# Kernel optimization log

Measured on AMD Instinct MI355X. Metric: run time of the kernel, lower is better.

## Reference

```python
import jax, jax.numpy as jnp
import numpy as np

N = 32
R = 128  # num_regions
F = 128  # num_features


def setup_inputs() -> dict:
    key = jax.random.key(0)
    k1, k2, k3, k4 = jax.random.split(key, 4)
    x1 = jax.random.normal(k1, (N, R * F), dtype=jnp.float32)
    x2 = jax.random.normal(k2, (N, R * F), dtype=jnp.float32)
    sigma = jax.random.normal(k3, (1,), dtype=jnp.float32) * 100.0
    mean = jax.random.normal(k4, (1,), dtype=jnp.float32)
    return {"x1": x1, "x2": x2, "sigma": sigma, "mean": mean}


def reference(x1, x2, sigma, mean):
    # (N, R, 1, F) - (N, 1, R, F) - mean -> (N, R, R, F)
    a = x1.reshape(N, R, 1, F)
    b = x2.reshape(N, 1, R, F)
    diff = a - b - mean  # mean is shape (1,), broadcasts over F
    distance_squared = jnp.sum(diff * diff, axis=-1)  # (N, R, R)
    kernel_value = jnp.exp(-distance_squared / (2.0 * sigma[0] ** 2))
    return jax.nn.softmax(kernel_value, axis=-1)
```

## Files before the change

### kernel.cpp

```cpp
#include <hip/hip_runtime.h>

#define NB 32
#define RR 128
#define FF 128
#define FT 32
#define SB 132

__global__ __launch_bounds__(256) void gauss_fused(const float* __restrict__ x1,
                                                   const float* __restrict__ x2,
                                                   const float* __restrict__ sigma,
                                                   const float* __restrict__ mean,
                                                   float* __restrict__ out) {
  __shared__ __align__(16) float sh_b[FT * SB];
  __shared__ __align__(16) float sh_a[8 * FF];

  const int bid = blockIdx.x;
  const int n = bid >> 4;
  const int i0 = (bid & 15) << 3;
  const int tid = threadIdx.x;
  const int tx = tid & 31;
  const int ty = tid >> 5;

  const float mval = mean[0];
  const float sg = sigma[0];
  const float cneg = -1.0f / (2.0f * sg * sg);

  {
    const float4 v = ((const float4*)(x1 + (size_t)(n * RR + i0) * FF))[tid];
    ((float4*)sh_a)[tid] = make_float4(v.x - mval, v.y - mval, v.z - mval, v.w - mval);
  }

  const float* __restrict__ x2base = x2 + (size_t)n * RR * FF;
  const int jj = tid >> 3;
  const int fo = (tid & 7) << 2;

  float acc0 = 0.f, acc1 = 0.f, acc2 = 0.f, acc3 = 0.f;
  const int j0 = tx << 2;
  const float* __restrict__ arow = sh_a + ty * FF;

  for (int t = 0; t < FF / FT; ++t) {
    const int ftw = t * FT;
    __syncthreads();
#pragma unroll
    for (int p = 0; p < 4; ++p) {
      const int j = jj + p * 32;
      const float4 v = *(const float4*)(x2base + (size_t)j * FF + ftw + fo);
      sh_b[(fo + 0) * SB + j] = v.x;
      sh_b[(fo + 1) * SB + j] = v.y;
      sh_b[(fo + 2) * SB + j] = v.z;
      sh_b[(fo + 3) * SB + j] = v.w;
    }
    __syncthreads();

#pragma unroll
    for (int f = 0; f < FT; ++f) {
      const float4 b = *(const float4*)(sh_b + f * SB + j0);
      const float a = arow[ftw + f];
      float d;
      d = a - b.x; acc0 = fmaf(d, d, acc0);
      d = a - b.y; acc1 = fmaf(d, d, acc1);
      d = a - b.z; acc2 = fmaf(d, d, acc2);
      d = a - b.w; acc3 = fmaf(d, d, acc3);
    }
  }

  const float k0 = __expf(acc0 * cneg);
  const float k1 = __expf(acc1 * cneg);
  const float k2 = __expf(acc2 * cneg);
  const float k3 = __expf(acc3 * cneg);

  float mx = fmaxf(fmaxf(k0, k1), fmaxf(k2, k3));
#pragma unroll
  for (int off = 16; off >= 1; off >>= 1) mx = fmaxf(mx, __shfl_xor(mx, off, 64));
  const float e0 = __expf(k0 - mx);
  const float e1 = __expf(k1 - mx);
  const float e2 = __expf(k2 - mx);
  const float e3 = __expf(k3 - mx);
  float ssum = e0 + e1 + e2 + e3;
#pragma unroll
  for (int off = 16; off >= 1; off >>= 1) ssum += __shfl_xor(ssum, off, 64);
  const float r = 1.0f / ssum;

  *(float4*)(out + (size_t)(n * RR + i0 + ty) * RR + j0) =
      make_float4(e0 * r, e1 * r, e2 * r, e3 * r);
}

extern "C" void kernel_launch(void* const* d_in, const int* in_sizes, int n_in,
                              void* d_out, int out_size, void* d_ws, size_t ws_size,
                              hipStream_t stream) {
  const float* x1 = (const float*)d_in[0];
  const float* x2 = (const float*)d_in[1];
  const float* sigma = (const float*)d_in[2];
  const float* mean = (const float*)d_in[3];
  float* out = (float*)d_out;
  (void)d_ws; (void)ws_size;

  gauss_fused<<<dim3(NB * 16), dim3(256), 0, stream>>>(x1, x2, sigma, mean, out);
}
```

Before: 69.42 us.

## Double-buffer x2 tiles in LDS with register prefetch and vectorized A reads

Turns the single shared-memory tile of x2 into two buffers. The next feature slice is prefetched into registers while the current slice is being computed, which overlaps the global-load latency with the math and cuts one barrier per iteration. It also reads the x1 row from shared memory as float4 vectors instead of scalars. The cost is more registers and twice the LDS for the B tile, which could lower occupancy.

```diff
diff --git a/kernel.cpp b/kernel.cpp
--- a/kernel.cpp
+++ b/kernel.cpp
@@ -11,7 +11,7 @@
                                                    const float* __restrict__ sigma,
                                                    const float* __restrict__ mean,
                                                    float* __restrict__ out) {
-  __shared__ __align__(16) float sh_b[FT * SB];
+  __shared__ __align__(16) float sh_b[2][FT * SB];
   __shared__ __align__(16) float sh_a[8 * FF];
 
   const int bid = blockIdx.x;
@@ -25,42 +25,87 @@
   const float sg = sigma[0];
   const float cneg = -1.0f / (2.0f * sg * sg);
 
+  const float* __restrict__ x2base = x2 + (size_t)n * RR * FF;
+  const int jj = tid >> 3;
+  const int fo = (tid & 7) << 2;
+
+  float4 p0 = *(const float4*)(x2base + (size_t)(jj + 0) * FF + fo);
+  float4 p1 = *(const float4*)(x2base + (size_t)(jj + 32) * FF + fo);
+  float4 p2 = *(const float4*)(x2base + (size_t)(jj + 64) * FF + fo);
+  float4 p3 = *(const float4*)(x2base + (size_t)(jj + 96) * FF + fo);
   {
     const float4 v = ((const float4*)(x1 + (size_t)(n * RR + i0) * FF))[tid];
     ((float4*)sh_a)[tid] = make_float4(v.x - mval, v.y - mval, v.z - mval, v.w - mval);
   }
-
-  const float* __restrict__ x2base = x2 + (size_t)n * RR * FF;
-  const int jj = tid >> 3;
-  const int fo = (tid & 7) << 2;
+  {
+    float* dst = sh_b[0];
+    dst[(fo + 0) * SB + (jj + 0)] = p0.x;
+    dst[(fo + 1) * SB + (jj + 0)] = p0.y;
+    dst[(fo + 2) * SB + (jj + 0)] = p0.z;
+    dst[(fo + 3) * SB + (jj + 0)] = p0.w;
+    dst[(fo + 0) * SB + (jj + 32)] = p1.x;
+    dst[(fo + 1) * SB + (jj + 32)] = p1.y;
+    dst[(fo + 2) * SB + (jj + 32)] = p1.z;
+    dst[(fo + 3) * SB + (jj + 32)] = p1.w;
+    dst[(fo + 0) * SB + (jj + 64)] = p2.x;
+    dst[(fo + 1) * SB + (jj + 64)] = p2.y;
+    dst[(fo + 2) * SB + (jj + 64)] = p2.z;
+    dst[(fo + 3) * SB + (jj + 64)] = p2.w;
+    dst[(fo + 0) * SB + (jj + 96)] = p3.x;
+    dst[(fo + 1) * SB + (jj + 96)] = p3.y;
+    dst[(fo + 2) * SB + (jj + 96)] = p3.z;
+    dst[(fo + 3) * SB + (jj + 96)] = p3.w;
+  }
+  __syncthreads();
 
   float acc0 = 0.f, acc1 = 0.f, acc2 = 0.f, acc3 = 0.f;
   const int j0 = tx << 2;
-  const float* __restrict__ arow = sh_a + ty * FF;
-
-  for (int t = 0; t < FF / FT; ++t) {
-    const int ftw = t * FT;
-    __syncthreads();
-#pragma unroll
-    for (int p = 0; p < 4; ++p) {
-      const int j = jj + p * 32;
-      const float4 v = *(const float4*)(x2base + (size_t)j * FF + ftw + fo);
-      sh_b[(fo + 0) * SB + j] = v.x;
-      sh_b[(fo + 1) * SB + j] = v.y;
-      sh_b[(fo + 2) * SB + j] = v.z;
-      sh_b[(fo + 3) * SB + j] = v.w;
-    }
-    __syncthreads();
+  int buf = 0;
 
 #pragma unroll
-    for (int f = 0; f < FT; ++f) {
-      const float4 b = *(const float4*)(sh_b + f * SB + j0);
-      const float a = arow[ftw + f];
-      float d;
-      d = a - b.x; acc0 = fmaf(d, d, acc0);
-      d = a - b.y; acc1 = fmaf(d, d, acc1);
-      d = a - b.z; acc2 = fmaf(d, d, acc2);
-      d = a - b.w; acc3 = fmaf(d, d, acc3);
+  for (int t = 0; t < FF / FT; ++t) {
+    float4 q[4];
+    if (t < 3) {
+      const float* src = x2base + (size_t)(t + 1) * FT + fo;
+#pragma unroll
+      for (int p = 0; p < 4; ++p)
+        q[p] = *(const float4*)(src + (size_t)(jj + 32 * p) * FF);
+    }
+
+    float4 a4[8];
+    {
+      const float4* asrc = (const float4*)(sh_a + ty * FF + t * FT);
+#pragma unroll
+      for (int fq = 0; fq < 8; ++fq) a4[fq] = asrc[fq];
+    }
+
+    const float* __restrict__ bb = sh_b[buf];
+#pragma unroll
+    for (int fq = 0; fq < 8; ++fq) {
+      const float4 av = a4[fq];
+#pragma unroll
+      for (int k = 0; k < 4; ++k) {
+        const float a = (k == 0) ? av.x : (k == 1) ? av.y : (k == 2) ? av.z : av.w;
+        const float4 b = *(const float4*)(bb + (fq * 4 + k) * SB + j0);
+        float d;
+        d = a - b.x; acc0 = fmaf(d, d, acc0);
+        d = a - b.y; acc1 = fmaf(d, d, acc1);
+        d = a - b.z; acc2 = fmaf(d, d, acc2);
+        d = a - b.w; acc3 = fmaf(d, d, acc3);
+      }
+    }
+
+    if (t < 3) {
+      float* dst = sh_b[buf ^ 1];
+#pragma unroll
+      for (int p = 0; p < 4; ++p) {
+        dst[(fo + 0) * SB + (jj + 32 * p)] = q[p].x;
+        dst[(fo + 1) * SB + (jj + 32 * p)] = q[p].y;
+        dst[(fo + 2) * SB + (jj + 32 * p)] = q[p].z;
+        dst[(fo + 3) * SB + (jj + 32 * p)] = q[p].w;
+      }
+      __syncthreads();
+      buf ^= 1;
     }
   }
 
```

Result: slower. 145.7 us (+109.8%).

## Stage full x2 slice once per block and compute two output rows per thread

Applied to the files above, without the earlier changes.

Each block now loads the whole 128x128 x2 slice for its batch into shared memory in one pass with a single barrier, replacing the four-chunk loop that synchronised twice per chunk. Each block handles 16 rows instead of 8, so each thread keeps two sets of accumulators and reuses every shared-memory b load for two rows. x1 values are read as float4 to cut LDS instructions. In exchange, shared memory grows to about 74KB per block and the grid halves to 256 blocks, which lowers occupancy and may leave some compute units idle on a large GPU.

```diff
diff --git a/kernel.cpp b/kernel.cpp
--- a/kernel.cpp
+++ b/kernel.cpp
@@ -3,7 +3,6 @@
 #define NB 32
 #define RR 128
 #define FF 128
-#define FT 32
 #define SB 132
 
 __global__ __launch_bounds__(256) void gauss_fused(const float* __restrict__ x1,
@@ -11,12 +10,12 @@
                                                    const float* __restrict__ sigma,
                                                    const float* __restrict__ mean,
                                                    float* __restrict__ out) {
-  __shared__ __align__(16) float sh_b[FT * SB];
-  __shared__ __align__(16) float sh_a[8 * FF];
+  __shared__ __align__(16) float sh_b[FF * SB];
+  __shared__ __align__(16) float sh_a[16 * FF];
 
   const int bid = blockIdx.x;
-  const int n = bid >> 4;
-  const int i0 = (bid & 15) << 3;
+  const int n = bid >> 3;
+  const int i0 = (bid & 7) << 4;
   const int tid = threadIdx.x;
   const int tx = tid & 31;
   const int ty = tid >> 5;
@@ -25,64 +24,98 @@
   const float sg = sigma[0];
   const float cneg = -1.0f / (2.0f * sg * sg);
 
+  const float* __restrict__ x2base = x2 + (size_t)n * RR * FF;
+
   {
-    const float4 v = ((const float4*)(x1 + (size_t)(n * RR + i0) * FF))[tid];
-    ((float4*)sh_a)[tid] = make_float4(v.x - mval, v.y - mval, v.z - mval, v.w - mval);
+    const float4* asrc = (const float4*)(x1 + (size_t)(n * RR + i0) * FF);
+    const float4 v0 = asrc[tid];
+    const float4 v1 = asrc[tid + 256];
+    ((float4*)sh_a)[tid] = make_float4(v0.x - mval, v0.y - mval, v0.z - mval, v0.w - mval);
+    ((float4*)sh_a)[tid + 256] = make_float4(v1.x - mval, v1.y - mval, v1.z - mval, v1.w - mval);
   }
 
-  const float* __restrict__ x2base = x2 + (size_t)n * RR * FF;
   const int jj = tid >> 3;
   const int fo = (tid & 7) << 2;
-
-  float acc0 = 0.f, acc1 = 0.f, acc2 = 0.f, acc3 = 0.f;
-  const int j0 = tx << 2;
-  const float* __restrict__ arow = sh_a + ty * FF;
-
-  for (int t = 0; t < FF / FT; ++t) {
-    const int ftw = t * FT;
-    __syncthreads();
+#pragma unroll
+  for (int fc = 0; fc < 4; ++fc) {
+    const int f0 = (fc << 5) + fo;
 #pragma unroll
     for (int p = 0; p < 4; ++p) {
-      const int j = jj + p * 32;
-      const float4 v = *(const float4*)(x2base + (size_t)j * FF + ftw + fo);
-      sh_b[(fo + 0) * SB + j] = v.x;
-      sh_b[(fo + 1) * SB + j] = v.y;
-      sh_b[(fo + 2) * SB + j] = v.z;
-      sh_b[(fo + 3) * SB + j] = v.w;
+      const int j = jj + (p << 5);
+      const float4 v = *(const float4*)(x2base + (size_t)j * FF + f0);
+      sh_b[(f0 + 0) * SB + j] = v.x;
+      sh_b[(f0 + 1) * SB + j] = v.y;
+      sh_b[(f0 + 2) * SB + j] = v.z;
+      sh_b[(f0 + 3) * SB + j] = v.w;
     }
-    __syncthreads();
+  }
+  __syncthreads();
 
+  float acc00 = 0.f, acc01 = 0.f, acc02 = 0.f, acc03 = 0.f;
+  float acc10 = 0.f, acc11 = 0.f, acc12 = 0.f, acc13 = 0.f;
+  const int j0 = tx << 2;
+  const float* __restrict__ arow0 = sh_a + ty * FF;
+  const float* __restrict__ arow1 = sh_a + (ty + 8) * FF;
+
+#pragma unroll 4
+  for (int fq = 0; fq < 32; ++fq) {
+    const float4 a0 = *(const float4*)(arow0 + (fq << 2));
+    const float4 a1 = *(const float4*)(arow1 + (fq << 2));
 #pragma unroll
-    for (int f = 0; f < FT; ++f) {
-      const float4 b = *(const float4*)(sh_b + f * SB + j0);
-      const float a = arow[ftw + f];
+    for (int c = 0; c < 4; ++c) {
+      const float4 b = *(const float4*)(sh_b + ((fq << 2) + c) * SB + j0);
+      const float a0c = (c == 0) ? a0.x : (c == 1) ? a0.y : (c == 2) ? a0.z : a0.w;
+      const float a1c = (c == 0) ? a1.x : (c == 1) ? a1.y : (c == 2) ? a1.z : a1.w;
       float d;
-      d = a - b.x; acc0 = fmaf(d, d, acc0);
-      d = a - b.y; acc1 = fmaf(d, d, acc1);
-      d = a - b.z; acc2 = fmaf(d, d, acc2);
-      d = a - b.w; acc3 = fmaf(d, d, acc3);
+      d = a0c - b.x; acc00 = fmaf(d, d, acc00);
+      d = a0c - b.y; acc01 = fmaf(d, d, acc01);
+      d = a0c - b.z; acc02 = fmaf(d, d, acc02);
+      d = a0c - b.w; acc03 = fmaf(d, d, acc03);
+      d = a1c - b.x; acc10 = fmaf(d, d, acc10);
+      d = a1c - b.y; acc11 = fmaf(d, d, acc11);
+      d = a1c - b.z; acc12 = fmaf(d, d, acc12);
+      d = a1c - b.w; acc13 = fmaf(d, d, acc13);
     }
   }
 
-  const float k0 = __expf(acc0 * cneg);
-  const float k1 = __expf(acc1 * cneg);
-  const float k2 = __expf(acc2 * cneg);
-  const float k3 = __expf(acc3 * cneg);
+  const float k00 = __expf(acc00 * cneg);
+  const float k01 = __expf(acc01 * cneg);
+  const float k02 = __expf(acc02 * cneg);
+  const float k03 = __expf(acc03 * cneg);
+  const float k10 = __expf(acc10 * cneg);
+  const float k11 = __expf(acc11 * cneg);
+  const float k12 = __expf(acc12 * cneg);
+  const float k13 = __expf(acc13 * cneg);
 
-  float mx = fmaxf(fmaxf(k0, k1), fmaxf(k2, k3));
+  float mx0 = fmaxf(fmaxf(k00, k01), fmaxf(k02, k03));
+  float mx1 = fmaxf(fmaxf(k10, k11), fmaxf(k12, k13));
 #pragma unroll
-  for (int off = 16; off >= 1; off >>= 1) mx = fmaxf(mx, __shfl_xor(mx, off, 64));
-  const float e0 = __expf(k0 - mx);
-  const float e1 = __expf(k1 - mx);
-  const float e2 = __expf(k2 - mx);
-  const float e3 = __expf(k3 - mx);
-  float ssum = e0 + e1 + e2 + e3;
+  for (int off = 16; off >= 1; off >>= 1) {
+    mx0 = fmaxf(mx0, __shfl_xor(mx0, off, 64));
+    mx1 = fmaxf(mx1, __shfl_xor(mx1, off, 64));
+  }
+  const float e00 = __expf(k00 - mx0);
+  const float e01 = __expf(k01 - mx0);
+  const float e02 = __expf(k02 - mx0);
+  const float e03 = __expf(k03 - mx0);
+  const float e10 = __expf(k10 - mx1);
+  const float e11 = __expf(k11 - mx1);
+  const float e12 = __expf(k12 - mx1);
+  const float e13 = __expf(k13 - mx1);
+  float s0 = e00 + e01 + e02 + e03;
+  float s1 = e10 + e11 + e12 + e13;
 #pragma unroll
-  for (int off = 16; off >= 1; off >>= 1) ssum += __shfl_xor(ssum, off, 64);
-  const float r = 1.0f / ssum;
+  for (int off = 16; off >= 1; off >>= 1) {
+    s0 += __shfl_xor(s0, off, 64);
+    s1 += __shfl_xor(s1, off, 64);
+  }
+  const float r0 = 1.0f / s0;
+  const float r1 = 1.0f / s1;
 
   *(float4*)(out + (size_t)(n * RR + i0 + ty) * RR + j0) =
-      make_float4(e0 * r, e1 * r, e2 * r, e3 * r);
+      make_float4(e00 * r0, e01 * r0, e02 * r0, e03 * r0);
+  *(float4*)(out + (size_t)(n * RR + i0 + ty + 8) * RR + j0) =
+      make_float4(e10 * r1, e11 * r1, e12 * r1, e13 * r1);
 }
 
 extern "C" void kernel_launch(void* const* d_in, const int* in_sizes, int n_in,
@@ -95,5 +128,5 @@
   float* out = (float*)d_out;
   (void)d_ws; (void)ws_size;
 
-  gauss_fused<<<dim3(NB * 16), dim3(256), 0, stream>>>(x1, x2, sigma, mean, out);
+  gauss_fused<<<dim3(NB * 8), dim3(256), 0, stream>>>(x1, x2, sigma, mean, out);
 }
```

Measured after the change: 68.62 us. About the same (-1.2%).

## Stage full x2 slice in shared memory once and remap blocks per XCD

Applied to the files above, without the earlier changes.

Each block now covers 16 rows with 512 threads and loads the whole 128x128 x2 slice for its batch into shared memory up front, with all global loads issued before any LDS stores. This replaces the four-stage load/sync loop with a single barrier. Block indices are remapped so that blocks of the same batch land on the same XCD, which should improve L2 reuse of x2. The x1 operand is now read as float4. In exchange the kernel uses about 76 KB of LDS per block and launches half as many blocks (256), which lowers occupancy and may leave some CUs idle.

```diff
diff --git a/kernel.cpp b/kernel.cpp
--- a/kernel.cpp
+++ b/kernel.cpp
@@ -3,20 +3,21 @@
 #define NB 32
 #define RR 128
 #define FF 128
-#define FT 32
 #define SB 132
 
-__global__ __launch_bounds__(256) void gauss_fused(const float* __restrict__ x1,
+__global__ __launch_bounds__(512) void gauss_fused(const float* __restrict__ x1,
                                                    const float* __restrict__ x2,
                                                    const float* __restrict__ sigma,
                                                    const float* __restrict__ mean,
                                                    float* __restrict__ out) {
-  __shared__ __align__(16) float sh_b[FT * SB];
-  __shared__ __align__(16) float sh_a[8 * FF];
+  __shared__ __align__(16) float sh_b[FF * SB];
+  __shared__ __align__(16) float sh_a[16 * FF];
 
-  const int bid = blockIdx.x;
-  const int n = bid >> 4;
-  const int i0 = (bid & 15) << 3;
+  const int d = blockIdx.x;
+  const int xcd = d & 7;
+  const int k = d >> 3;
+  const int n = (xcd << 2) + (k >> 3);
+  const int i0 = (k & 7) << 4;
   const int tid = threadIdx.x;
   const int tx = tid & 31;
   const int ty = tid >> 5;
@@ -25,42 +26,50 @@
   const float sg = sigma[0];
   const float cneg = -1.0f / (2.0f * sg * sg);
 
-  {
-    const float4 v = ((const float4*)(x1 + (size_t)(n * RR + i0) * FF))[tid];
-    ((float4*)sh_a)[tid] = make_float4(v.x - mval, v.y - mval, v.z - mval, v.w - mval);
+  const float* __restrict__ x2base = x2 + (size_t)n * RR * FF;
+
+  const int jj = (tid >> 3) & 31;
+  const int fo = (tid & 7) << 2;
+  const int hb = (tid >> 8) << 6;
+
+#define LDQ(fc, p) \
+  *(const float4*)(x2base + (size_t)(jj + ((p) << 5)) * FF + hb + ((fc) << 5) + fo)
+  const float4 q00 = LDQ(0, 0), q01 = LDQ(0, 1), q02 = LDQ(0, 2), q03 = LDQ(0, 3);
+  const float4 q10 = LDQ(1, 0), q11 = LDQ(1, 1), q12 = LDQ(1, 2), q13 = LDQ(1, 3);
+#undef LDQ
+  const float4 va = ((const float4*)(x1 + (size_t)(n * RR + i0) * FF))[tid];
+
+  ((float4*)sh_a)[tid] = make_float4(va.x - mval, va.y - mval, va.z - mval, va.w - mval);
+#define STW(q, fc, p)                                 \
+  {                                                   \
+    const int f0 = hb + ((fc) << 5) + fo;             \
+    const int j = jj + ((p) << 5);                    \
+    sh_b[(f0 + 0) * SB + j] = (q).x;                  \
+    sh_b[(f0 + 1) * SB + j] = (q).y;                  \
+    sh_b[(f0 + 2) * SB + j] = (q).z;                  \
+    sh_b[(f0 + 3) * SB + j] = (q).w;                  \
   }
-
-  const float* __restrict__ x2base = x2 + (size_t)n * RR * FF;
-  const int jj = tid >> 3;
-  const int fo = (tid & 7) << 2;
+  STW(q00, 0, 0) STW(q01, 0, 1) STW(q02, 0, 2) STW(q03, 0, 3)
+  STW(q10, 1, 0) STW(q11, 1, 1) STW(q12, 1, 2) STW(q13, 1, 3)
+#undef STW
+  __syncthreads();
 
   float acc0 = 0.f, acc1 = 0.f, acc2 = 0.f, acc3 = 0.f;
   const int j0 = tx << 2;
   const float* __restrict__ arow = sh_a + ty * FF;
 
-  for (int t = 0; t < FF / FT; ++t) {
-    const int ftw = t * FT;
-    __syncthreads();
+#pragma unroll 4
+  for (int fq = 0; fq < 32; ++fq) {
+    const float4 a = *(const float4*)(arow + (fq << 2));
 #pragma unroll
-    for (int p = 0; p < 4; ++p) {
-      const int j = jj + p * 32;
-      const float4 v = *(const float4*)(x2base + (size_t)j * FF + ftw + fo);
-      sh_b[(fo + 0) * SB + j] = v.x;
-      sh_b[(fo + 1) * SB + j] = v.y;
-      sh_b[(fo + 2) * SB + j] = v.z;
-      sh_b[(fo + 3) * SB + j] = v.w;
-    }
-    __syncthreads();
-
-#pragma unroll
-    for (int f = 0; f < FT; ++f) {
-      const float4 b = *(const float4*)(sh_b + f * SB + j0);
-      const float a = arow[ftw + f];
-      float d;
-      d = a - b.x; acc0 = fmaf(d, d, acc0);
-      d = a - b.y; acc1 = fmaf(d, d, acc1);
-      d = a - b.z; acc2 = fmaf(d, d, acc2);
-      d = a - b.w; acc3 = fmaf(d, d, acc3);
+    for (int c = 0; c < 4; ++c) {
+      const float4 b = *(const float4*)(sh_b + ((fq << 2) + c) * SB + j0);
+      const float ac = (c == 0) ? a.x : (c == 1) ? a.y : (c == 2) ? a.z : a.w;
+      float dd;
+      dd = ac - b.x; acc0 = fmaf(dd, dd, acc0);
+      dd = ac - b.y; acc1 = fmaf(dd, dd, acc1);
+      dd = ac - b.z; acc2 = fmaf(dd, dd, acc2);
+      dd = ac - b.w; acc3 = fmaf(dd, dd, acc3);
     }
   }
 
@@ -95,5 +104,5 @@
   float* out = (float*)d_out;
   (void)d_ws; (void)ws_size;
 
-  gauss_fused<<<dim3(NB * 16), dim3(256), 0, stream>>>(x1, x2, sigma, mean, out);
+  gauss_fused<<<dim3(NB * 8), dim3(512), 0, stream>>>(x1, x2, sigma, mean, out);
 }
```

Result: faster. 66.13 us (-4.8%).
